# Performance work log

Measured on AMD Instinct MI355X. Metric: run time of the kernel, lower is better.

## Reference

```python
import jax, jax.numpy as jnp
import numpy as np

N_NODES = 50000
N_EDGES = 800000
IN_F = 128
HID = 128


def _sage_mean(x, edge_src, edge_dst, W_self, W_neigh, b, n_nodes):
    # DGL SAGEConv('mean'): out = x @ W_self^T + mean_{in-neighbors}(x_src) @ W_neigh^T + b
    msg = x[edge_src]                                        # [E, F] gather
    agg = jax.ops.segment_sum(msg, edge_dst, num_segments=n_nodes)
    deg = jax.ops.segment_sum(jnp.ones((edge_dst.shape[0],), x.dtype), edge_dst,
                              num_segments=n_nodes)
    h_neigh = agg / jnp.maximum(deg, 1.0)[:, None]           # zero-in-degree -> 0
    return x @ W_self.T + h_neigh @ W_neigh.T + b


def setup_inputs() -> dict:
    key = jax.random.key(0)
    ks = jax.random.split(key, 10)
    s = 1.0 / np.sqrt(HID)
    return {
        "x": jax.random.normal(ks[0], (N_NODES, IN_F), jnp.float32),
        "edge_src": jax.random.randint(ks[1], (N_EDGES,), 0, N_NODES, jnp.int32),
        "edge_dst": jax.random.randint(ks[2], (N_EDGES,), 0, N_NODES, jnp.int32),
        "states": jax.random.randint(ks[3], (256,), 0, N_NODES, jnp.int32),
        "actions": jax.random.randint(ks[4], (1,), 0, N_NODES, jnp.int32),
        "W1_self": jax.random.normal(ks[5], (HID, IN_F), jnp.float32) * s,
        "W1_neigh": jax.random.normal(ks[6], (HID, IN_F), jnp.float32) * s,
        "b1": jnp.zeros((HID,), jnp.float32),
        "W2_self": jax.random.normal(ks[7], (HID, HID), jnp.float32) * s,
        "W2_neigh": jax.random.normal(ks[8], (HID, HID), jnp.float32) * s,
        "b2": jnp.zeros((HID,), jnp.float32),
        "Wfc": jax.random.normal(ks[9], (1, 2 * HID), jnp.float32) * s,
        "bfc": jnp.zeros((1,), jnp.float32),
    }


def reference(x, edge_src, edge_dst, states, actions,
              W1_self, W1_neigh, b1, W2_self, W2_neigh, b2, Wfc, bfc):
    n = x.shape[0]
    h = jax.nn.relu(_sage_mean(x, edge_src, edge_dst, W1_self, W1_neigh, b1, n))
    # dropout(p=0.1) is identity at inference
    h = jax.nn.relu(_sage_mean(h, edge_src, edge_dst, W2_self, W2_neigh, b2, n))
    states_vec = h[states]                                   # [S, HID]
    actions_vec = h[actions]                                 # [1, HID]
    states_agg = jnp.max(states_vec, axis=0, keepdims=True)  # [1, HID]
    hcat = jnp.concatenate([states_agg, actions_vec], axis=1)  # [1, 2*HID]
    return hcat @ Wfc.T + bfc                                # [1, 1]
```

## Files before the change

kernel.cpp:

```cpp
#include <hip/hip_runtime.h>

#define NN 50000
#define NE 800000
#define FD 128
#define L1CAP 16000
#define BCAP 64
#define BMW 1564
#define POISON_I ((int)0xAAAAAAAA)

#define GS 16
#define LDSTR 132
#define WCH 16
#define WSTR 20



__global__ __launch_bounds__(256) void k_scanT(
        const int4* __restrict__ edst4, const int4* __restrict__ esrc4,
        const int* __restrict__ states, const int* __restrict__ actions,
        unsigned* __restrict__ fbm, int* __restrict__ nodeL1,
        int* __restrict__ cnt) {
    __shared__ unsigned sbm[BMW];
    int tid = threadIdx.x;
    for (int w = tid; w < BMW; w += 256) sbm[w] = 0u;
    __syncthreads();
    for (int i = tid; i < 257; i += 256) {
        int n = (i < 256) ? states[i] : actions[0];
        atomicOr(&sbm[n >> 5], 1u << (n & 31));
    }
    __syncthreads();

    int lane = tid & 63;
    int t = blockIdx.x * 256 + tid;
    int fresh[4];
    int nd[4];
#pragma unroll
    for (int j = 0; j < 4; ++j) { fresh[j] = 0; nd[j] = 0; }

    if (t < NE / 4) {
        int4 d4 = edst4[t];
        int hit0 = (sbm[d4.x >> 5] >> (d4.x & 31)) & 1;
        int hit1 = (sbm[d4.y >> 5] >> (d4.y & 31)) & 1;
        int hit2 = (sbm[d4.z >> 5] >> (d4.z & 31)) & 1;
        int hit3 = (sbm[d4.w >> 5] >> (d4.w & 31)) & 1;
        if (hit0 | hit1 | hit2 | hit3) {
            int4 s4 = esrc4[t];
            int hs[4] = {hit0, hit1, hit2, hit3};
            int ss[4] = {s4.x, s4.y, s4.z, s4.w};
#pragma unroll
            for (int j = 0; j < 4; ++j) {
                if (hs[j]) {
                    int n = ss[j];
                    unsigned bit = 1u << (n & 31);
                    unsigned old = (n & 1)
                        ? atomicAnd(&fbm[n >> 5], ~bit)
                        : atomicOr(&fbm[n >> 5], bit);
                    fresh[j] = (((old & bit) != 0u) == ((n & 1) != 0));
                    nd[j] = n;
                }
            }
        }
    }

#pragma unroll
    for (int j = 0; j < 4; ++j) {
        unsigned long long m = __ballot(fresh[j]);
        if (m) {
            int lead = __ffsll(m) - 1;
            int c = __popcll(m);
            int basep = 0;
            if (lane == lead) basep = atomicAdd(&cnt[0], c);
            basep = __shfl(basep, lead, 64);
            if (fresh[j]) {
                int pos = basep - POISON_I +
                          __popcll(m & ((1ull << lane) - 1ull));
                if ((unsigned)pos < L1CAP) nodeL1[pos] = nd[j];
            }
        }
    }

    if (blockIdx.x == 0) {
        for (int i = tid; i < 257; i += 256) {
            int n = (i < 256) ? states[i] : actions[0];
            unsigned bit = 1u << (n & 31);
            unsigned old = (n & 1)
                ? atomicAnd(&fbm[n >> 5], ~bit)
                : atomicOr(&fbm[n >> 5], bit);
            if (((old & bit) != 0u) == ((n & 1) != 0)) {
                int pos = atomicAdd(&cnt[0], 1) - POISON_I;
                if ((unsigned)pos < L1CAP) nodeL1[pos] = n;
            }
        }
    }
}


__global__ __launch_bounds__(256) void k_scanL1(
        const int4* __restrict__ edst4, const int4* __restrict__ esrc4,
        const unsigned* __restrict__ fbm, int* __restrict__ cur1,
        int* __restrict__ bsrc1) {
    __shared__ unsigned sbm[BMW];
    for (int w = threadIdx.x; w < BMW; w += 256) sbm[w] = fbm[w];
    __syncthreads();
    int t = blockIdx.x * 256 + threadIdx.x;
    if (t >= NE / 4) return;
    int4 d4 = edst4[t];
    int h0 = ((sbm[d4.x >> 5] >> (d4.x & 31)) ^ d4.x) & 1;
    int h1_ = ((sbm[d4.y >> 5] >> (d4.y & 31)) ^ d4.y) & 1;
    int h2 = ((sbm[d4.z >> 5] >> (d4.z & 31)) ^ d4.z) & 1;
    int h3 = ((sbm[d4.w >> 5] >> (d4.w & 31)) ^ d4.w) & 1;
    if (!(h0 | h1_ | h2 | h3)) return;
    int4 s4 = esrc4[t];
    int hs[4] = {h0, h1_, h2, h3};
    int ds[4] = {d4.x, d4.y, d4.z, d4.w};
    int ss[4] = {s4.x, s4.y, s4.z, s4.w};
#pragma unroll
    for (int j = 0; j < 4; ++j) {
        if (hs[j]) {
            int d = ds[j];
            int pos = atomicAdd(&cur1[d], 1) - POISON_I;
            if ((unsigned)pos < BCAP) bsrc1[(size_t)d * BCAP + pos] = ss[j];
        }
    }
}


__global__ __launch_bounds__(256, 2) void k_gemm1(
        const float* __restrict__ x, const int* __restrict__ nodeL1,
        const int* __restrict__ cur1, const int* __restrict__ bsrc1,
        const int* __restrict__ cntPtr,
        const float* __restrict__ Wself, const float* __restrict__ Wneigh,
        const float* __restrict__ bias, float* __restrict__ h1) {
    __shared__ float sx[GS][LDSTR];
    __shared__ float sa[GS][LDSTR];
    __shared__ float swS[FD][WSTR];
    __shared__ float swN[FD][WSTR];
    int cnt = *cntPtr - POISON_I;
    if (cnt < 0) cnt = 0;
    if (cnt > L1CAP) cnt = L1CAP;
    int base = blockIdx.x * GS;
    if (base >= cnt) return;
    int tid = threadIdx.x, lane = tid & 63, wv = tid >> 6;

    for (int s = wv; s < GS; s += 4) {
        int slot = base + s;
        int node = 0, nt = 0;
        if (slot < cnt) {
            node = nodeL1[slot];
            if ((unsigned)node >= NN) node = 0;
            nt = cur1[node] - POISON_I;
            if (nt < 0) nt = 0;
        }
        float2 xv = ((const float2*)(x + (size_t)node * FD))[lane];
        ((float2*)&sx[s][0])[lane] = xv;
        int n = nt > BCAP ? BCAP : nt;
        const int* bp = bsrc1 + (size_t)node * BCAP;
        float ax = 0.0f, ay = 0.0f;
        int e = 0;
        for (; e + 3 < n; e += 4) {
            int r0 = bp[e], r1 = bp[e + 1], r2 = bp[e + 2], r3 = bp[e + 3];
            if ((unsigned)r0 >= NN) r0 = 0;
            if ((unsigned)r1 >= NN) r1 = 0;
            if ((unsigned)r2 >= NN) r2 = 0;
            if ((unsigned)r3 >= NN) r3 = 0;
            float2 v0 = ((const float2*)(x + (size_t)r0 * FD))[lane];
            float2 v1 = ((const float2*)(x + (size_t)r1 * FD))[lane];
            float2 v2 = ((const float2*)(x + (size_t)r2 * FD))[lane];
            float2 v3 = ((const float2*)(x + (size_t)r3 * FD))[lane];
            ax += (v0.x + v1.x) + (v2.x + v3.x);
            ay += (v0.y + v1.y) + (v2.y + v3.y);
        }
        for (; e < n; ++e) {
            int r = bp[e];
            if ((unsigned)r >= NN) r = 0;
            float2 v = ((const float2*)(x + (size_t)r * FD))[lane];
            ax += v.x; ay += v.y;
        }
        float inv = 1.0f / fmaxf((float)nt, 1.0f);
        float2 av; av.x = ax * inv; av.y = ay * inv;
        ((float2*)&sa[s][0])[lane] = av;
    }
    __syncthreads();

    int og = tid & 15;
    int sg = tid >> 4;
    float acc[8];
#pragma unroll
    for (int j = 0; j < 8; ++j) acc[j] = 0.0f;

    for (int kb = 0; kb < FD; kb += WCH) {
#pragma unroll
        for (int i = 0; i < 2; ++i) {
            int idx = tid + 256 * i;
            int o = idx >> 2, c4 = (idx & 3) * 4;
            *(float4*)&swS[o][c4] = *(const float4*)(Wself + (size_t)o * FD + kb + c4);
            *(float4*)&swN[o][c4] = *(const float4*)(Wneigh + (size_t)o * FD + kb + c4);
        }
        __syncthreads();
#pragma unroll
        for (int k = 0; k < WCH; k += 4) {
            float4 xv = *(const float4*)&sx[sg][kb + k];
            float4 av = *(const float4*)&sa[sg][kb + k];
#pragma unroll
            for (int j = 0; j < 8; ++j) {
                int o = og + 16 * j;
                float4 ws = *(const float4*)&swS[o][k];
                float4 wn = *(const float4*)&swN[o][k];
                acc[j] += xv.x * ws.x + xv.y * ws.y + xv.z * ws.z + xv.w * ws.w
                        + av.x * wn.x + av.y * wn.y + av.z * wn.z + av.w * wn.w;
            }
        }
        __syncthreads();
    }

    int slot = base + sg;
    if (slot < cnt) {
        int srow = nodeL1[slot];
        if ((unsigned)srow >= NN) srow = 0;
#pragma unroll
        for (int j = 0; j < 8; ++j) {
            int o = og + 16 * j;
            h1[(size_t)srow * FD + o] = fmaxf(acc[j] + bias[o], 0.0f);
        }
    }
}


__global__ __launch_bounds__(256, 2) void k_gemm2(
        const float* __restrict__ h1,
        const int* __restrict__ states, const int* __restrict__ actions,
        const int* __restrict__ cur1, const int* __restrict__ bsrc1,
        const float* __restrict__ Wself, const float* __restrict__ Wneigh,
        const float* __restrict__ bias,
        const float* __restrict__ Wfc, const float* __restrict__ bfc,
        int* __restrict__ smax, float* __restrict__ actRow,
        int* __restrict__ done, float* __restrict__ out) {
    __shared__ float sx[GS][LDSTR];
    __shared__ float sa[GS][LDSTR];
    __shared__ float swS[FD][WSTR];
    __shared__ float swN[FD][WSTR];
    __shared__ int lmax[FD];
    const int cnt = 257;
    int base = blockIdx.x * GS;
    int tid = threadIdx.x, lane = tid & 63, wv = tid >> 6;

    if (tid < FD) lmax[tid] = 0;

    for (int s = wv; s < GS; s += 4) {
        int slot = base + s;
        int node, nt = 0;
        if (slot < 256) node = states[slot];
        else if (slot == 256) node = actions[0];
        else node = -1;
        if (node >= 0) {
            if ((unsigned)node >= NN) node = 0;
            nt = cur1[node] - POISON_I;
            if (nt < 0) nt = 0;
        } else {
            node = 0;
        }
        float2 xv = ((const float2*)(h1 + (size_t)node * FD))[lane];
        ((float2*)&sx[s][0])[lane] = xv;
        int n = nt > BCAP ? BCAP : nt;
        const int* bp = bsrc1 + (size_t)node * BCAP;
        float ax = 0.0f, ay = 0.0f;
        int e = 0;
        for (; e + 3 < n; e += 4) {
            int r0 = bp[e], r1 = bp[e + 1], r2 = bp[e + 2], r3 = bp[e + 3];
            if ((unsigned)r0 >= NN) r0 = 0;
            if ((unsigned)r1 >= NN) r1 = 0;
            if ((unsigned)r2 >= NN) r2 = 0;
            if ((unsigned)r3 >= NN) r3 = 0;
            float2 v0 = ((const float2*)(h1 + (size_t)r0 * FD))[lane];
            float2 v1 = ((const float2*)(h1 + (size_t)r1 * FD))[lane];
            float2 v2 = ((const float2*)(h1 + (size_t)r2 * FD))[lane];
            float2 v3 = ((const float2*)(h1 + (size_t)r3 * FD))[lane];
            ax += (v0.x + v1.x) + (v2.x + v3.x);
            ay += (v0.y + v1.y) + (v2.y + v3.y);
        }
        for (; e < n; ++e) {
            int r = bp[e];
            if ((unsigned)r >= NN) r = 0;
            float2 v = ((const float2*)(h1 + (size_t)r * FD))[lane];
            ax += v.x; ay += v.y;
        }
        float inv = 1.0f / fmaxf((float)nt, 1.0f);
        float2 av; av.x = ax * inv; av.y = ay * inv;
        ((float2*)&sa[s][0])[lane] = av;
    }
    __syncthreads();

    int og = tid & 15;
    int sg = tid >> 4;
    float acc[8];
#pragma unroll
    for (int j = 0; j < 8; ++j) acc[j] = 0.0f;

    for (int kb = 0; kb < FD; kb += WCH) {
#pragma unroll
        for (int i = 0; i < 2; ++i) {
            int idx = tid + 256 * i;
            int o = idx >> 2, c4 = (idx & 3) * 4;
            *(float4*)&swS[o][c4] = *(const float4*)(Wself + (size_t)o * FD + kb + c4);
            *(float4*)&swN[o][c4] = *(const float4*)(Wneigh + (size_t)o * FD + kb + c4);
        }
        __syncthreads();
#pragma unroll
        for (int k = 0; k < WCH; k += 4) {
            float4 xv = *(const float4*)&sx[sg][kb + k];
            float4 av = *(const float4*)&sa[sg][kb + k];
#pragma unroll
            for (int j = 0; j < 8; ++j) {
                int o = og + 16 * j;
                float4 ws = *(const float4*)&swS[o][k];
                float4 wn = *(const float4*)&swN[o][k];
                acc[j] += xv.x * ws.x + xv.y * ws.y + xv.z * ws.z + xv.w * ws.w
                        + av.x * wn.x + av.y * wn.y + av.z * wn.z + av.w * wn.w;
            }
        }
        __syncthreads();
    }

    int slot = base + sg;
#pragma unroll
    for (int j = 0; j < 8; ++j) {
        int o = og + 16 * j;
        float v = fmaxf(acc[j] + bias[o], 0.0f);
        if (slot < 256) atomicMax(&lmax[o], __float_as_int(v));
        else if (slot == 256) actRow[o] = v;
    }
    __syncthreads();
    if (tid < FD) atomicMax(&smax[tid], lmax[tid]);

    __shared__ int amLast;
    __syncthreads();
    if (tid == 0) {
        __threadfence();
        amLast = (atomicAdd(done, 1) == POISON_I + (int)gridDim.x - 1);
    }
    __syncthreads();
    if (!amLast) return;
    __threadfence();

    __shared__ float red[256];
    float v = 0.0f;
    if (tid < FD)
        v = __int_as_float(smax[tid]) * Wfc[tid] + actRow[tid] * Wfc[FD + tid];
    red[tid] = v;
    __syncthreads();
    for (int sr = 128; sr > 0; sr >>= 1) {
        if (tid < sr) red[tid] += red[tid + sr];
        __syncthreads();
    }
    if (tid == 0) out[0] = red[0] + bfc[0];
    (void)cnt;
}


extern "C" void kernel_launch(void* const* d_in, const int* in_sizes, int n_in,
                              void* d_out, int out_size, void* d_ws, size_t ws_size,
                              hipStream_t stream) {
    (void)in_sizes; (void)n_in; (void)out_size; (void)ws_size;
    const float* x    = (const float*)d_in[0];
    const int4* esrc4 = (const int4*)d_in[1];
    const int4* edst4 = (const int4*)d_in[2];
    const int* states = (const int*)d_in[3];
    const int* acts   = (const int*)d_in[4];
    const float* W1s  = (const float*)d_in[5];
    const float* W1n  = (const float*)d_in[6];
    const float* b1   = (const float*)d_in[7];
    const float* W2s  = (const float*)d_in[8];
    const float* W2n  = (const float*)d_in[9];
    const float* b2   = (const float*)d_in[10];
    const float* Wfc  = (const float*)d_in[11];
    const float* bfc  = (const float*)d_in[12];
    float* out = (float*)d_out;

    char* ws = (char*)d_ws;
    size_t o = 0;
    auto take = [&](size_t sz) {
        size_t r = o;
        o = (o + sz + 255) & ~(size_t)255;
        return r;
    };
    size_t off_cnt    = take(256);
    size_t off_smax   = take(FD * 4);
    size_t off_act    = take(FD * 4);
    size_t off_done   = take(256);
    size_t off_fbm    = take((size_t)BMW * 4);
    size_t off_nodeL1 = take((size_t)L1CAP * 4);
    size_t off_cur1   = take((size_t)NN * 4);
    size_t off_bsrc1  = take((size_t)NN * BCAP * 4);
    size_t off_h1     = take((size_t)NN * FD * 4);

    int*      cnt    = (int*)(ws + off_cnt);
    int*      smax   = (int*)(ws + off_smax);
    float*    actRow = (float*)(ws + off_act);
    int*      done1  = (int*)(ws + off_done);
    unsigned* fbm    = (unsigned*)(ws + off_fbm);
    int*      nodeL1 = (int*)(ws + off_nodeL1);
    int*      cur1   = (int*)(ws + off_cur1);
    int*      bsrc1  = (int*)(ws + off_bsrc1);
    float*    h1     = (float*)(ws + off_h1);

    int scanBlocks = (NE / 4 + 255) / 256;

    k_scanT<<<scanBlocks, 256, 0, stream>>>(edst4, esrc4, states, acts,
                                            fbm, nodeL1, cnt);
    k_scanL1<<<scanBlocks, 256, 0, stream>>>(edst4, esrc4, fbm, cur1, bsrc1);
    k_gemm1<<<L1CAP / GS, 256, 0, stream>>>(x, nodeL1, cur1, bsrc1, cnt,
                                            W1s, W1n, b1, h1);
    k_gemm2<<<(257 + GS - 1) / GS, 256, 0, stream>>>(
        h1, states, acts, cur1, bsrc1, W2s, W2n, b2, Wfc, bfc,
        smax, actRow, done1, out);
}
```

Measured before the change: 215.0 us.

## Split neighbor gather from GEMM into separate kernels, widen GEMM tile to 32 rows

Mean-neighbor aggregation moves out of the fused gather+GEMM kernels into dedicated grid-stride gather kernels that write compacted aggregates to a workspace buffer. The gather loads each wave's neighbor indices once per lane and broadcasts them with shuffles instead of reloading them per edge. The GEMM kernels now process 32 rows per block with two accumulator rows per thread, so each weight tile staged in shared memory is reused twice as much. In exchange, two extra launches and an extra round trip of the aggregates through global memory are added.

```diff
diff --git a/kernel.cpp b/kernel.cpp
--- a/kernel.cpp
+++ b/kernel.cpp
@@ -8,7 +8,7 @@
 #define BMW 1564
 #define POISON_I ((int)0xAAAAAAAA)
 
-#define GS 16
+#define GSLOTS 32
 #define LDSTR 132
 #define WCH 16
 #define WSTR 20
@@ -125,44 +125,35 @@
 }
 
 
-__global__ __launch_bounds__(256, 2) void k_gemm1(
-        const float* __restrict__ x, const int* __restrict__ nodeL1,
-        const int* __restrict__ cur1, const int* __restrict__ bsrc1,
-        const int* __restrict__ cntPtr,
-        const float* __restrict__ Wself, const float* __restrict__ Wneigh,
-        const float* __restrict__ bias, float* __restrict__ h1) {
-    __shared__ float sx[GS][LDSTR];
-    __shared__ float sa[GS][LDSTR];
-    __shared__ float swS[FD][WSTR];
-    __shared__ float swN[FD][WSTR];
+__global__ __launch_bounds__(256) void k_gather1(
+        const int* __restrict__ nodeL1, const int* __restrict__ cur1,
+        const int* __restrict__ bsrc1, const int* __restrict__ cntPtr,
+        const float* __restrict__ x, float* __restrict__ agg1c) {
+    int lane = threadIdx.x & 63;
+    int wid = (blockIdx.x * blockDim.x + threadIdx.x) >> 6;
+    int nwv = (gridDim.x * blockDim.x) >> 6;
     int cnt = *cntPtr - POISON_I;
     if (cnt < 0) cnt = 0;
     if (cnt > L1CAP) cnt = L1CAP;
-    int base = blockIdx.x * GS;
-    if (base >= cnt) return;
-    int tid = threadIdx.x, lane = tid & 63, wv = tid >> 6;
-
-    for (int s = wv; s < GS; s += 4) {
-        int slot = base + s;
-        int node = 0, nt = 0;
-        if (slot < cnt) {
-            node = nodeL1[slot];
-            if ((unsigned)node >= NN) node = 0;
-            nt = cur1[node] - POISON_I;
-            if (nt < 0) nt = 0;
-        }
-        float2 xv = ((const float2*)(x + (size_t)node * FD))[lane];
-        ((float2*)&sx[s][0])[lane] = xv;
+    for (int w = wid; w < cnt; w += nwv) {
+        int node = nodeL1[w];
+        if ((unsigned)node >= NN) node = 0;
+        int nt = cur1[node] - POISON_I;
+        if (nt < 0) nt = 0;
         int n = nt > BCAP ? BCAP : nt;
         const int* bp = bsrc1 + (size_t)node * BCAP;
+        int myidx = 0;
+        if (lane < n) {
+            myidx = bp[lane];
+            if ((unsigned)myidx >= NN) myidx = 0;
+        }
         float ax = 0.0f, ay = 0.0f;
         int e = 0;
         for (; e + 3 < n; e += 4) {
-            int r0 = bp[e], r1 = bp[e + 1], r2 = bp[e + 2], r3 = bp[e + 3];
-            if ((unsigned)r0 >= NN) r0 = 0;
-            if ((unsigned)r1 >= NN) r1 = 0;
-            if ((unsigned)r2 >= NN) r2 = 0;
-            if ((unsigned)r3 >= NN) r3 = 0;
+            int r0 = __shfl(myidx, e, 64);
+            int r1 = __shfl(myidx, e + 1, 64);
+            int r2 = __shfl(myidx, e + 2, 64);
+            int r3 = __shfl(myidx, e + 3, 64);
             float2 v0 = ((const float2*)(x + (size_t)r0 * FD))[lane];
             float2 v1 = ((const float2*)(x + (size_t)r1 * FD))[lane];
             float2 v2 = ((const float2*)(x + (size_t)r2 * FD))[lane];
@@ -171,22 +162,69 @@
             ay += (v0.y + v1.y) + (v2.y + v3.y);
         }
         for (; e < n; ++e) {
-            int r = bp[e];
-            if ((unsigned)r >= NN) r = 0;
+            int r = __shfl(myidx, e, 64);
             float2 v = ((const float2*)(x + (size_t)r * FD))[lane];
             ax += v.x; ay += v.y;
         }
         float inv = 1.0f / fmaxf((float)nt, 1.0f);
-        float2 av; av.x = ax * inv; av.y = ay * inv;
-        ((float2*)&sa[s][0])[lane] = av;
+        float2 outv; outv.x = ax * inv; outv.y = ay * inv;
+        ((float2*)(agg1c + (size_t)w * FD))[lane] = outv;
+    }
+}
+
+
+__global__ __launch_bounds__(256, 2) void k_gemm1(
+        const float* __restrict__ x, const int* __restrict__ nodeL1,
+        const float* __restrict__ agg1c,
+        const float* __restrict__ Wself, const float* __restrict__ Wneigh,
+        const float* __restrict__ bias, float* __restrict__ h1,
+        const int* __restrict__ cntPtr) {
+    __shared__ float sx[GSLOTS][LDSTR];
+    __shared__ float sa[GSLOTS][LDSTR];
+    __shared__ float swS[FD][WSTR];
+    __shared__ float swN[FD][WSTR];
+    __shared__ int   srowL[GSLOTS];
+    int cnt = *cntPtr - POISON_I;
+    if (cnt < 0) cnt = 0;
+    if (cnt > L1CAP) cnt = L1CAP;
+    int base = blockIdx.x * GSLOTS;
+    if (base >= cnt) return;
+    int tid = threadIdx.x;
+
+    if (tid < GSLOTS) {
+        int slot = base + tid;
+        int srow = (slot < cnt) ? nodeL1[slot] : 0;
+        if ((unsigned)srow >= NN) srow = 0;
+        srowL[tid] = srow;
+    }
+    __syncthreads();
+
+    {
+        int c4 = tid & 31;
+        int r0 = tid >> 5;
+        float4 rx[4], ra[4];
+#pragma unroll
+        for (int i = 0; i < 4; ++i) {
+            int r = r0 + 8 * i;
+            rx[i] = ((const float4*)(x + (size_t)srowL[r] * FD))[c4];
+            ra[i] = ((const float4*)(agg1c + (size_t)(base + r) * FD))[c4];
+        }
+#pragma unroll
+        for (int i = 0; i < 4; ++i) {
+            int r = r0 + 8 * i;
+            *(float4*)&sx[r][c4 * 4] = rx[i];
+            *(float4*)&sa[r][c4 * 4] = ra[i];
+        }
     }
     __syncthreads();
 
     int og = tid & 15;
     int sg = tid >> 4;
-    float acc[8];
-#pragma unroll
-    for (int j = 0; j < 8; ++j) acc[j] = 0.0f;
+    float acc[2][8];
+#pragma unroll
+    for (int i = 0; i < 2; ++i)
+#pragma unroll
+        for (int j = 0; j < 8; ++j) acc[i][j] = 0.0f;
 
     for (int kb = 0; kb < FD; kb += WCH) {
 #pragma unroll
@@ -199,78 +237,68 @@
         __syncthreads();
 #pragma unroll
         for (int k = 0; k < WCH; k += 4) {
-            float4 xv = *(const float4*)&sx[sg][kb + k];
-            float4 av = *(const float4*)&sa[sg][kb + k];
+            float4 xv[2], av[2];
+#pragma unroll
+            for (int i = 0; i < 2; ++i) {
+                int s = sg + 16 * i;
+                xv[i] = *(const float4*)&sx[s][kb + k];
+                av[i] = *(const float4*)&sa[s][kb + k];
+            }
 #pragma unroll
             for (int j = 0; j < 8; ++j) {
                 int o = og + 16 * j;
                 float4 ws = *(const float4*)&swS[o][k];
                 float4 wn = *(const float4*)&swN[o][k];
-                acc[j] += xv.x * ws.x + xv.y * ws.y + xv.z * ws.z + xv.w * ws.w
-                        + av.x * wn.x + av.y * wn.y + av.z * wn.z + av.w * wn.w;
+#pragma unroll
+                for (int i = 0; i < 2; ++i) {
+                    acc[i][j] += xv[i].x * ws.x + xv[i].y * ws.y + xv[i].z * ws.z + xv[i].w * ws.w
+                               + av[i].x * wn.x + av[i].y * wn.y + av[i].z * wn.z + av[i].w * wn.w;
+                }
             }
         }
         __syncthreads();
     }
 
-    int slot = base + sg;
-    if (slot < cnt) {
-        int srow = nodeL1[slot];
-        if ((unsigned)srow >= NN) srow = 0;
-#pragma unroll
-        for (int j = 0; j < 8; ++j) {
-            int o = og + 16 * j;
-            h1[(size_t)srow * FD + o] = fmaxf(acc[j] + bias[o], 0.0f);
-        }
-    }
-}
-
-
-__global__ __launch_bounds__(256, 2) void k_gemm2(
-        const float* __restrict__ h1,
+#pragma unroll
+    for (int j = 0; j < 8; ++j) {
+        int o = og + 16 * j;
+        float b = bias[o];
+#pragma unroll
+        for (int i = 0; i < 2; ++i) {
+            int r = sg + 16 * i;
+            if (base + r < cnt)
+                h1[(size_t)srowL[r] * FD + o] = fmaxf(acc[i][j] + b, 0.0f);
+        }
+    }
+}
+
+
+__global__ __launch_bounds__(256) void k_gather2(
         const int* __restrict__ states, const int* __restrict__ actions,
         const int* __restrict__ cur1, const int* __restrict__ bsrc1,
-        const float* __restrict__ Wself, const float* __restrict__ Wneigh,
-        const float* __restrict__ bias,
-        const float* __restrict__ Wfc, const float* __restrict__ bfc,
-        int* __restrict__ smax, float* __restrict__ actRow,
-        int* __restrict__ done, float* __restrict__ out) {
-    __shared__ float sx[GS][LDSTR];
-    __shared__ float sa[GS][LDSTR];
-    __shared__ float swS[FD][WSTR];
-    __shared__ float swN[FD][WSTR];
-    __shared__ int lmax[FD];
-    const int cnt = 257;
-    int base = blockIdx.x * GS;
-    int tid = threadIdx.x, lane = tid & 63, wv = tid >> 6;
-
-    if (tid < FD) lmax[tid] = 0;
-
-    for (int s = wv; s < GS; s += 4) {
-        int slot = base + s;
-        int node, nt = 0;
-        if (slot < 256) node = states[slot];
-        else if (slot == 256) node = actions[0];
-        else node = -1;
-        if (node >= 0) {
-            if ((unsigned)node >= NN) node = 0;
-            nt = cur1[node] - POISON_I;
-            if (nt < 0) nt = 0;
-        } else {
-            node = 0;
-        }
-        float2 xv = ((const float2*)(h1 + (size_t)node * FD))[lane];
-        ((float2*)&sx[s][0])[lane] = xv;
+        const float* __restrict__ h1, float* __restrict__ agg2c) {
+    int lane = threadIdx.x & 63;
+    int wid = (blockIdx.x * blockDim.x + threadIdx.x) >> 6;
+    int nwv = (gridDim.x * blockDim.x) >> 6;
+    for (int w = wid; w < 257; w += nwv) {
+        int node = (w < 256) ? states[w] : actions[0];
+        if ((unsigned)node >= NN) node = 0;
+        int nt = cur1[node] - POISON_I;
+        if (nt < 0) nt = 0;
         int n = nt > BCAP ? BCAP : nt;
         const int* bp = bsrc1 + (size_t)node * BCAP;
+        int myidx = 0;
+        if (lane < n) {
+            myidx = bp[lane];
+            if ((unsigned)myidx >= NN) myidx = 0;
+        }
         float ax = 0.0f, ay = 0.0f;
         int e = 0;
         for (; e + 3 < n; e += 4) {
-            int r0 = bp[e], r1 = bp[e + 1], r2 = bp[e + 2], r3 = bp[e + 3];
-            if ((unsigned)r0 >= NN) r0 = 0;
-            if ((unsigned)r1 >= NN) r1 = 0;
-            if ((unsigned)r2 >= NN) r2 = 0;
-            if ((unsigned)r3 >= NN) r3 = 0;
+            int r0 = __shfl(myidx, e, 64);
+            int r1 = __shfl(myidx, e + 1, 64);
+            int r2 = __shfl(myidx, e + 2, 64);
+            int r3 = __shfl(myidx, e + 3, 64);
             float2 v0 = ((const float2*)(h1 + (size_t)r0 * FD))[lane];
             float2 v1 = ((const float2*)(h1 + (size_t)r1 * FD))[lane];
             float2 v2 = ((const float2*)(h1 + (size_t)r2 * FD))[lane];
@@ -279,22 +307,74 @@
             ay += (v0.y + v1.y) + (v2.y + v3.y);
         }
         for (; e < n; ++e) {
-            int r = bp[e];
-            if ((unsigned)r >= NN) r = 0;
+            int r = __shfl(myidx, e, 64);
             float2 v = ((const float2*)(h1 + (size_t)r * FD))[lane];
             ax += v.x; ay += v.y;
         }
         float inv = 1.0f / fmaxf((float)nt, 1.0f);
-        float2 av; av.x = ax * inv; av.y = ay * inv;
-        ((float2*)&sa[s][0])[lane] = av;
+        float2 outv; outv.x = ax * inv; outv.y = ay * inv;
+        ((float2*)(agg2c + (size_t)w * FD))[lane] = outv;
+    }
+}
+
+
+__global__ __launch_bounds__(256, 2) void k_gemm2(
+        const float* __restrict__ h1,
+        const int* __restrict__ states, const int* __restrict__ actions,
+        const float* __restrict__ agg2c,
+        const float* __restrict__ Wself, const float* __restrict__ Wneigh,
+        const float* __restrict__ bias,
+        const float* __restrict__ Wfc, const float* __restrict__ bfc,
+        int* __restrict__ smax, float* __restrict__ actRow,
+        int* __restrict__ done, float* __restrict__ out) {
+    __shared__ float sx[GSLOTS][LDSTR];
+    __shared__ float sa[GSLOTS][LDSTR];
+    __shared__ float swS[FD][WSTR];
+    __shared__ float swN[FD][WSTR];
+    __shared__ int   srowL[GSLOTS];
+    __shared__ int   lmax[FD];
+    const int cnt = 257;
+    int base = blockIdx.x * GSLOTS;
+    int tid = threadIdx.x;
+
+    if (tid < FD) lmax[tid] = 0;
+    if (tid < GSLOTS) {
+        int slot = base + tid;
+        int node;
+        if (slot < 256) node = states[slot];
+        else if (slot == 256) node = actions[0];
+        else node = states[0];
+        if ((unsigned)node >= NN) node = 0;
+        srowL[tid] = node;
+    }
+    __syncthreads();
+
+    {
+        int c4 = tid & 31;
+        int r0 = tid >> 5;
+        float4 rx[4], ra[4];
+#pragma unroll
+        for (int i = 0; i < 4; ++i) {
+            int r = r0 + 8 * i;
+            rx[i] = ((const float4*)(h1 + (size_t)srowL[r] * FD))[c4];
+            ra[i] = ((const float4*)(agg2c + (size_t)(base + r) * FD))[c4];
+        }
+#pragma unroll
+        for (int i = 0; i < 4; ++i) {
+            int r = r0 + 8 * i;
+            *(float4*)&sx[r][c4 * 4] = rx[i];
+            *(float4*)&sa[r][c4 * 4] = ra[i];
+        }
     }
     __syncthreads();
 
     int og = tid & 15;
     int sg = tid >> 4;
-    float acc[8];
-#pragma unroll
-    for (int j = 0; j < 8; ++j) acc[j] = 0.0f;
+    float acc[2][8];
+#pragma unroll
+    for (int i = 0; i < 2; ++i)
+#pragma unroll
+        for (int j = 0; j < 8; ++j) acc[i][j] = 0.0f;
 
     for (int kb = 0; kb < FD; kb += WCH) {
 #pragma unroll
@@ -307,27 +387,39 @@
         __syncthreads();
 #pragma unroll
         for (int k = 0; k < WCH; k += 4) {
-            float4 xv = *(const float4*)&sx[sg][kb + k];
-            float4 av = *(const float4*)&sa[sg][kb + k];
+            float4 xv[2], av[2];
+#pragma unroll
+            for (int i = 0; i < 2; ++i) {
+                int s = sg + 16 * i;
+                xv[i] = *(const float4*)&sx[s][kb + k];
+                av[i] = *(const float4*)&sa[s][kb + k];
+            }
 #pragma unroll
             for (int j = 0; j < 8; ++j) {
                 int o = og + 16 * j;
                 float4 ws = *(const float4*)&swS[o][k];
                 float4 wn = *(const float4*)&swN[o][k];
-                acc[j] += xv.x * ws.x + xv.y * ws.y + xv.z * ws.z + xv.w * ws.w
-                        + av.x * wn.x + av.y * wn.y + av.z * wn.z + av.w * wn.w;
+#pragma unroll
+                for (int i = 0; i < 2; ++i) {
+                    acc[i][j] += xv[i].x * ws.x + xv[i].y * ws.y + xv[i].z * ws.z + xv[i].w * ws.w
+                               + av[i].x * wn.x + av[i].y * wn.y + av[i].z * wn.z + av[i].w * wn.w;
+                }
             }
         }
         __syncthreads();
     }
 
-    int slot = base + sg;
 #pragma unroll
     for (int j = 0; j < 8; ++j) {
         int o = og + 16 * j;
-        float v = fmaxf(acc[j] + bias[o], 0.0f);
-        if (slot < 256) atomicMax(&lmax[o], __float_as_int(v));
-        else if (slot == 256) actRow[o] = v;
+        float b = bias[o];
+#pragma unroll
+        for (int i = 0; i < 2; ++i) {
+            int slot = base + sg + 16 * i;
+            float v = fmaxf(acc[i][j] + b, 0.0f);
+            if (slot < 256) atomicMax(&lmax[o], __float_as_int(v));
+            else if (slot == 256) actRow[o] = v;
+        }
     }
     __syncthreads();
     if (tid < FD) atomicMax(&smax[tid], lmax[tid]);
@@ -391,6 +483,8 @@
     size_t off_nodeL1 = take((size_t)L1CAP * 4);
     size_t off_cur1   = take((size_t)NN * 4);
     size_t off_bsrc1  = take((size_t)NN * BCAP * 4);
+    size_t off_agg1c  = take((size_t)L1CAP * FD * 4);
+    size_t off_agg2c  = take((size_t)512 * FD * 4);
     size_t off_h1     = take((size_t)NN * FD * 4);
 
     int*      cnt    = (int*)(ws + off_cnt);
@@ -401,6 +495,8 @@
     int*      nodeL1 = (int*)(ws + off_nodeL1);
     int*      cur1   = (int*)(ws + off_cur1);
     int*      bsrc1  = (int*)(ws + off_bsrc1);
+    float*    agg1c  = (float*)(ws + off_agg1c);
+    float*    agg2c  = (float*)(ws + off_agg2c);
     float*    h1     = (float*)(ws + off_h1);
 
     int scanBlocks = (NE / 4 + 255) / 256;
@@ -408,9 +504,11 @@
     k_scanT<<<scanBlocks, 256, 0, stream>>>(edst4, esrc4, states, acts,
                                             fbm, nodeL1, cnt);
     k_scanL1<<<scanBlocks, 256, 0, stream>>>(edst4, esrc4, fbm, cur1, bsrc1);
-    k_gemm1<<<L1CAP / GS, 256, 0, stream>>>(x, nodeL1, cur1, bsrc1, cnt,
-                                            W1s, W1n, b1, h1);
-    k_gemm2<<<(257 + GS - 1) / GS, 256, 0, stream>>>(
-        h1, states, acts, cur1, bsrc1, W2s, W2n, b2, Wfc, bfc,
+    k_gather1<<<1536, 256, 0, stream>>>(nodeL1, cur1, bsrc1, cnt, x, agg1c);
+    k_gemm1<<<L1CAP / GSLOTS, 256, 0, stream>>>(x, nodeL1, agg1c,
+                                                W1s, W1n, b1, h1, cnt);
+    k_gather2<<<128, 256, 0, stream>>>(states, acts, cur1, bsrc1, h1, agg2c);
+    k_gemm2<<<(257 + GSLOTS - 1) / GSLOTS, 256, 0, stream>>>(
+        h1, states, acts, agg2c, W2s, W2n, b2, Wfc, bfc,
         smax, actRow, done1, out);
 }
```

Result: faster. 201.0 us (-6.5%).
